# Optimization experiments

Hardware: AMD Instinct MI355X
Metric: run time of the kernel (lower is better)

The kernel has to match this reference:

```python
import jax, jax.numpy as jnp
import numpy as np

B, S, D = 2, 2048, 640
H, DH = 8, 80  # heads, dim_head
SCALE = DH ** -0.5


def setup_inputs() -> dict:
    key = jax.random.key(0)
    ks = jax.random.split(key, 7)
    std = D ** -0.5
    return {
        "x": jax.random.normal(ks[0], (B, S, D), jnp.float32),
        "encoder_hidden_states": jax.random.normal(ks[1], (B, S, D), jnp.float32),
        # Linear weights stored as [in, out] so application is x @ W
        "Wq": jax.random.normal(ks[2], (D, H * DH), jnp.float32) * std,
        "Wk": jax.random.normal(ks[3], (D, H * DH), jnp.float32) * std,
        "Wv": jax.random.normal(ks[4], (D, H * DH), jnp.float32) * std,
        "Wo": jax.random.normal(ks[5], (H * DH, D), jnp.float32) * std,
        "bo": jax.random.normal(ks[6], (D,), jnp.float32) * 0.01,
    }


def reference(x, encoder_hidden_states, Wq, Wk, Wv, Wo, bo):
    # projections (to_q/to_k/to_v have bias=False)
    q = x @ Wq                      # [B, S, H*DH]
    k = encoder_hidden_states @ Wk  # [B, S, H*DH]
    v = encoder_hidden_states @ Wv  # [B, S, H*DH]

    def split_heads(t):
        b, s, _ = t.shape
        return t.reshape(b, s, H, DH).transpose(0, 2, 1, 3)  # [B, H, S, DH]

    q, k, v = split_heads(q), split_heads(k), split_heads(v)

    # the torch loop over bh-chunks computes plain softmax attention; same math fused
    scores = jnp.einsum("bhid,bhjd->bhij", q, k) * SCALE  # [B, H, Sq, Skv]
    attn = jax.nn.softmax(scores, axis=-1)
    out = jnp.einsum("bhij,bhjd->bhid", attn, v)          # [B, H, Sq, DH]

    out = out.transpose(0, 2, 1, 3).reshape(x.shape[0], x.shape[1], H * DH)
    return out @ Wo + bo  # to_out[0]; Dropout(p=0) is identity
```

## Files before the change

kernel.cpp:

```cpp
#include <hip/hip_runtime.h>
#include <hip/hip_bf16.h>

typedef __bf16 v4bf __attribute__((ext_vector_type(4)));
typedef __bf16 v8bf __attribute__((ext_vector_type(8)));
typedef float  v4f  __attribute__((ext_vector_type(4)));

namespace {
constexpr int Bb  = 2;
constexpr int Ss  = 2048;
constexpr int Dd  = 640;
constexpr int Hh  = 8;
constexpr int DHh = 80;
constexpr int Mm  = Bb * Ss;
constexpr float kQScale = 0.11180339887498949f * 1.4426950408889634f;

__device__ __forceinline__ float4 ld4(const float* p) {
  return *reinterpret_cast<const float4*>(p);
}
}

__global__ __launch_bounds__(256)
void wtrans_kernel(const float* __restrict__ Wq, const float* __restrict__ Wk,
                   const float* __restrict__ Wv, const float* __restrict__ Wo,
                   __bf16* __restrict__ Wtq, __bf16* __restrict__ Wtk,
                   __bf16* __restrict__ Wtv, __bf16* __restrict__ Wto) {
  const int z = blockIdx.z;
  const float* W = (z == 0) ? Wq : (z == 1) ? Wk : (z == 2) ? Wv : Wo;
  __bf16* Wt = (z == 0) ? Wtq : (z == 1) ? Wtk : (z == 2) ? Wtv : Wto;
  const int k0 = blockIdx.y * 32, n0 = blockIdx.x * 32;
  __shared__ float t[32][33];
  const int tid = threadIdx.x;
  {
    int kr = tid >> 3, c4 = (tid & 7) * 4;
    float4 f = ld4(W + (size_t)(k0 + kr) * Dd + n0 + c4);
    t[kr][c4 + 0] = f.x; t[kr][c4 + 1] = f.y;
    t[kr][c4 + 2] = f.z; t[kr][c4 + 3] = f.w;
  }
  __syncthreads();
  {
    int nr = tid >> 3, kc = (tid & 7) * 4;
    v4bf p;
#pragma unroll
    for (int u = 0; u < 4; ++u) p[u] = (__bf16)t[kc + u][nr];
    *reinterpret_cast<v4bf*>(&Wt[(size_t)(n0 + nr) * Dd + k0 + kc]) = p;
  }
}

template <bool AF32>
__device__ __forceinline__ void gemm_core_db(const void* __restrict__ Ap,
                                             const __bf16* __restrict__ Bt,
                                             __bf16* As, __bf16* Bs, int m0,
                                             int n0, int rh, int ch,
                                             v4f acc[4][4]) {
  constexpr int BUF = 128 * 40;
  constexpr int NKB = Dd / 32;
  const int tid = threadIdx.x;
  const int lane = tid & 63;
  const int quad = lane >> 4, l15 = lane & 15;
  const int lr = tid >> 1;
  const int lk = (tid & 1) * 16;
  const __bf16* Bg = Bt + (size_t)(n0 + lr) * Dd + lk;
  const float* Af = (const float*)Ap;
  const __bf16* Ab = (const __bf16*)Ap;

#pragma unroll
  for (int i = 0; i < 4; ++i)
#pragma unroll
    for (int j = 0; j < 4; ++j) acc[i][j] = (v4f){0.f, 0.f, 0.f, 0.f};

  v8bf a0, a1, b0, b1;
  if constexpr (AF32) {
    const float* ap = Af + (size_t)(m0 + lr) * Dd + lk;
    float4 f0 = ld4(ap), f1 = ld4(ap + 4), f2 = ld4(ap + 8), f3 = ld4(ap + 12);
    a0[0]=(__bf16)f0.x; a0[1]=(__bf16)f0.y; a0[2]=(__bf16)f0.z; a0[3]=(__bf16)f0.w;
    a0[4]=(__bf16)f1.x; a0[5]=(__bf16)f1.y; a0[6]=(__bf16)f1.z; a0[7]=(__bf16)f1.w;
    a1[0]=(__bf16)f2.x; a1[1]=(__bf16)f2.y; a1[2]=(__bf16)f2.z; a1[3]=(__bf16)f2.w;
    a1[4]=(__bf16)f3.x; a1[5]=(__bf16)f3.y; a1[6]=(__bf16)f3.z; a1[7]=(__bf16)f3.w;
  } else {
    const __bf16* ap = Ab + (size_t)(m0 + lr) * Dd + lk;
    a0 = *reinterpret_cast<const v8bf*>(ap);
    a1 = *reinterpret_cast<const v8bf*>(ap + 8);
  }
  b0 = *reinterpret_cast<const v8bf*>(Bg);
  b1 = *reinterpret_cast<const v8bf*>(Bg + 8);
  *reinterpret_cast<v8bf*>(&As[lr * 40 + lk])     = a0;
  *reinterpret_cast<v8bf*>(&As[lr * 40 + lk + 8]) = a1;
  *reinterpret_cast<v8bf*>(&Bs[lr * 40 + lk])     = b0;
  *reinterpret_cast<v8bf*>(&Bs[lr * 40 + lk + 8]) = b1;

  for (int it = 0; it < NKB; ++it) {
    if (it + 1 < NKB) {
      const int kb = (it + 1) * 32;
      if constexpr (AF32) {
        const float* ap = Af + (size_t)(m0 + lr) * Dd + kb + lk;
        float4 f0 = ld4(ap), f1 = ld4(ap + 4), f2 = ld4(ap + 8),
               f3 = ld4(ap + 12);
        a0[0]=(__bf16)f0.x; a0[1]=(__bf16)f0.y; a0[2]=(__bf16)f0.z; a0[3]=(__bf16)f0.w;
        a0[4]=(__bf16)f1.x; a0[5]=(__bf16)f1.y; a0[6]=(__bf16)f1.z; a0[7]=(__bf16)f1.w;
        a1[0]=(__bf16)f2.x; a1[1]=(__bf16)f2.y; a1[2]=(__bf16)f2.z; a1[3]=(__bf16)f2.w;
        a1[4]=(__bf16)f3.x; a1[5]=(__bf16)f3.y; a1[6]=(__bf16)f3.z; a1[7]=(__bf16)f3.w;
      } else {
        const __bf16* ap = Ab + (size_t)(m0 + lr) * Dd + kb + lk;
        a0 = *reinterpret_cast<const v8bf*>(ap);
        a1 = *reinterpret_cast<const v8bf*>(ap + 8);
      }
      b0 = *reinterpret_cast<const v8bf*>(Bg + kb);
      b1 = *reinterpret_cast<const v8bf*>(Bg + kb + 8);
    }
    __syncthreads();
    const int cur = (it & 1) * BUF, nxt = BUF - cur;
    v8bf af[4], bv[4];
#pragma unroll
    for (int i = 0; i < 4; ++i)
      af[i] = *reinterpret_cast<const v8bf*>(
          &As[cur + (rh + i * 16 + l15) * 40 + quad * 8]);
#pragma unroll
    for (int j = 0; j < 4; ++j)
      bv[j] = *reinterpret_cast<const v8bf*>(
          &Bs[cur + (ch + j * 16 + l15) * 40 + quad * 8]);
#pragma unroll
    for (int i = 0; i < 4; ++i)
#pragma unroll
      for (int j = 0; j < 4; ++j)
        acc[i][j] = __builtin_amdgcn_mfma_f32_16x16x32_bf16(af[i], bv[j],
                                                            acc[i][j], 0, 0, 0);
    if (it + 1 < NKB) {
      *reinterpret_cast<v8bf*>(&As[nxt + lr * 40 + lk])     = a0;
      *reinterpret_cast<v8bf*>(&As[nxt + lr * 40 + lk + 8]) = a1;
      *reinterpret_cast<v8bf*>(&Bs[nxt + lr * 40 + lk])     = b0;
      *reinterpret_cast<v8bf*>(&Bs[nxt + lr * 40 + lk + 8]) = b1;
    }
  }
}

__global__ __launch_bounds__(256)
void gemm_qkv_mfma(const float* __restrict__ x, const float* __restrict__ ehs,
                   const __bf16* __restrict__ Wtq,
                   const __bf16* __restrict__ Wtk,
                   const __bf16* __restrict__ Wtv, __bf16* __restrict__ qb,
                   __bf16* __restrict__ kbuf, __bf16* __restrict__ vb) {
  const int z = blockIdx.z;
  const float* A = (z == 0) ? x : ehs;
  const __bf16* Bt = (z == 0) ? Wtq : (z == 1) ? Wtk : Wtv;
  __bf16* C = (z == 0) ? qb : (z == 1) ? kbuf : vb;
  const float scale = (z == 0) ? kQScale : 1.0f;

  __shared__ __bf16 As[2 * 128 * 40];
  __shared__ __bf16 Bs[2 * 128 * 40];
  const int tid = threadIdx.x;
  const int w = tid >> 6, lane = tid & 63;
  const int quad = lane >> 4, l15 = lane & 15;
  const int m0 = blockIdx.y * 128, n0 = blockIdx.x * 128;
  const int rh = (w >> 1) * 64, ch = (w & 1) * 64;
  v4f acc[4][4];
  gemm_core_db<true>(A, Bt, As, Bs, m0, n0, rh, ch, acc);

  if (z == 2) {
#pragma unroll
    for (int i = 0; i < 4; ++i)
#pragma unroll
      for (int j = 0; j < 4; ++j) {
        int m = m0 + rh + i * 16 + quad * 4;
        int n = n0 + ch + j * 16 + l15;
        int bb = m >> 11, tok = m & 2047;
        v4bf pk;
#pragma unroll
        for (int r = 0; r < 4; ++r) pk[r] = (__bf16)acc[i][j][r];
        *reinterpret_cast<v4bf*>(&C[((size_t)bb * Dd + n) * Ss + tok]) = pk;
      }
  } else {
#pragma unroll
    for (int i = 0; i < 4; ++i)
#pragma unroll
      for (int j = 0; j < 4; ++j) {
        int m = m0 + rh + i * 16 + quad * 4;
        int n = n0 + ch + j * 16 + l15;
#pragma unroll
        for (int r = 0; r < 4; ++r)
          C[(size_t)(m + r) * Dd + n] = (__bf16)(acc[i][j][r] * scale);
      }
  }
}

__global__ __launch_bounds__(256)
void gemm_out_mfma(const __bf16* __restrict__ A, const __bf16* __restrict__ Bt,
                   const float* __restrict__ bias, float* __restrict__ out) {
  __shared__ __bf16 As[2 * 128 * 40];
  __shared__ __bf16 Bs[2 * 128 * 40];
  const int tid = threadIdx.x;
  const int w = tid >> 6, lane = tid & 63;
  const int quad = lane >> 4, l15 = lane & 15;
  const int m0 = blockIdx.y * 128, n0 = blockIdx.x * 128;
  const int rh = (w >> 1) * 64, ch = (w & 1) * 64;
  v4f acc[4][4];
  gemm_core_db<false>(A, Bt, As, Bs, m0, n0, rh, ch, acc);

#pragma unroll
  for (int i = 0; i < 4; ++i)
#pragma unroll
    for (int j = 0; j < 4; ++j) {
      int m = m0 + rh + i * 16 + quad * 4;
      int n = n0 + ch + j * 16 + l15;
      float bn = bias[n];
#pragma unroll
      for (int r = 0; r < 4; ++r)
        out[(size_t)(m + r) * Dd + n] = acc[i][j][r] + bn;
    }
}

__global__ __launch_bounds__(256, 2)
void attn_mfma_kernel(const __bf16* __restrict__ q,
                      const __bf16* __restrict__ k,
                      const __bf16* __restrict__ vtg, __bf16* __restrict__ o) {
  constexpr int QT = 64;
  constexpr int KT = 32;
  constexpr int KW = Ss / 4;
  constexpr int NIT = KW / KT;
  constexpr int LQ = 104;
  constexpr int LV = 40;
  constexpr int KS = KT * LQ;
  constexpr int VS = 96 * LV;
  constexpr int PS = QT * LV;
  constexpr int WSZ = KS + VS + PS;
  constexpr int LM = 100;

  __shared__ __align__(16) __bf16 smem[4 * WSZ];

  const int bh = blockIdx.y;
  const int b = bh >> 3, h = bh & 7;
  const int q0 = blockIdx.x * QT;
  const int tid = threadIdx.x;
  const int w = tid >> 6;
  const int lane = tid & 63;
  const int quad = lane >> 4;
  const int l15 = lane & 15;

  __bf16* ksw = smem + w * WSZ;
  __bf16* vtw = ksw + KS;
  __bf16* psw = vtw + VS;

  const __bf16* qg  = q + (size_t)(b * Ss + q0) * Dd + h * DHh;
  const __bf16* kgb = k + (size_t)(b * Ss) * Dd + h * DHh;
  const __bf16* vgb = vtg + ((size_t)b * Dd + h * DHh) * Ss;

  v8bf qf[4][3];
#pragma unroll
  for (int qt = 0; qt < 4; ++qt)
#pragma unroll
    for (int s = 0; s < 3; ++s) {
      if (s == 2 && quad >= 2) {
        qf[qt][s] = (v8bf){};
      } else {
        qf[qt][s] = *reinterpret_cast<const v8bf*>(
            qg + (size_t)(qt * 16 + l15) * Dd + s * 32 + quad * 8);
      }
    }

  const int kgo = (lane >> 1) * Dd + (lane & 1) * 4;
  const int klo = (lane >> 1) * LQ + (lane & 1) * 4;
  const int vgo = (lane >> 2) * Ss + (lane & 3) * 8;
  const int vlo = (lane >> 2) * LV + (lane & 3) * 8;

  {
    v8bf z8 = {};
    *reinterpret_cast<v8bf*>(&ksw[(lane >> 1) * LQ + 80 + (lane & 1) * 8]) = z8;
    v8bf pad = {};
    int vr = 80 + (lane >> 2);
    if (vr == 80) {
#pragma unroll
      for (int e = 0; e < 8; ++e) pad[e] = (__bf16)1.f;
    }
    *reinterpret_cast<v8bf*>(&vtw[vr * LV + (lane & 3) * 8]) = pad;
  }
  {
    const __bf16* kg = kgb + (size_t)(w * KW) * Dd;
#pragma unroll
    for (int c = 0; c < 10; ++c)
      *reinterpret_cast<v4bf*>(&ksw[klo + c * 8]) =
          *reinterpret_cast<const v4bf*>(kg + kgo + c * 8);
  }

  v4f Oacc[4][6];
#pragma unroll
  for (int qt = 0; qt < 4; ++qt)
#pragma unroll
    for (int mt = 0; mt < 6; ++mt) Oacc[qt][mt] = (v4f){0.f, 0.f, 0.f, 0.f};

  for (int it = 0; it < NIT; ++it) {
    const bool pfK = (it + 1 < NIT);
    v4bf kreg[10];
    if (pfK) {
      const __bf16* kg = kgb + (size_t)(w * KW + (it + 1) * KT) * Dd;
#pragma unroll
      for (int c = 0; c < 10; ++c)
        kreg[c] = *reinterpret_cast<const v4bf*>(kg + kgo + c * 8);
    }

    v4f sacc[4][2];
#pragma unroll
    for (int qt = 0; qt < 4; ++qt) {
      sacc[qt][0] = (v4f){0.f, 0.f, 0.f, 0.f};
      sacc[qt][1] = (v4f){0.f, 0.f, 0.f, 0.f};
    }
    __builtin_amdgcn_s_setprio(1);
#pragma unroll
    for (int s = 0; s < 3; ++s) {
      v8bf ak0 = *reinterpret_cast<const v8bf*>(
          &ksw[l15 * LQ + s * 32 + quad * 8]);
      v8bf ak1 = *reinterpret_cast<const v8bf*>(
          &ksw[(16 + l15) * LQ + s * 32 + quad * 8]);
#pragma unroll
      for (int qt = 0; qt < 4; ++qt) {
        sacc[qt][0] = __builtin_amdgcn_mfma_f32_16x16x32_bf16(
            ak0, qf[qt][s], sacc[qt][0], 0, 0, 0);
        sacc[qt][1] = __builtin_amdgcn_mfma_f32_16x16x32_bf16(
            ak1, qf[qt][s], sacc[qt][1], 0, 0, 0);
      }
    }

    v8bf vreg[5];
    {
      const __bf16* vg = vgb + (w * KW + it * KT);
#pragma unroll
      for (int c = 0; c < 5; ++c)
        vreg[c] = *reinterpret_cast<const v8bf*>(vg + vgo +
                                                 (size_t)c * 16 * Ss);
    }

    if (it > 0) {
      v8bf bp[4];
#pragma unroll
      for (int qt = 0; qt < 4; ++qt)
        bp[qt] = *reinterpret_cast<const v8bf*>(
            &psw[(qt * 16 + l15) * LV + quad * 8]);
#pragma unroll
      for (int mt = 0; mt < 6; ++mt) {
        v8bf av = *reinterpret_cast<const v8bf*>(
            &vtw[(mt * 16 + l15) * LV + quad * 8]);
#pragma unroll
        for (int qt = 0; qt < 4; ++qt)
          Oacc[qt][mt] = __builtin_amdgcn_mfma_f32_16x16x32_bf16(
              av, bp[qt], Oacc[qt][mt], 0, 0, 0);
      }
    }
    __builtin_amdgcn_s_setprio(0);

#pragma unroll
    for (int qt = 0; qt < 4; ++qt)
#pragma unroll
      for (int mt = 0; mt < 2; ++mt) {
        v4bf pk;
#pragma unroll
        for (int r = 0; r < 4; ++r) pk[r] = (__bf16)exp2f(sacc[qt][mt][r]);
        *reinterpret_cast<v4bf*>(
            &psw[(qt * 16 + l15) * LV + mt * 16 + quad * 4]) = pk;
      }

    if (pfK) {
#pragma unroll
      for (int c = 0; c < 10; ++c)
        *reinterpret_cast<v4bf*>(&ksw[klo + c * 8]) = kreg[c];
    }
#pragma unroll
    for (int c = 0; c < 5; ++c)
      *reinterpret_cast<v8bf*>(&vtw[vlo + c * 16 * LV]) = vreg[c];
  }

  {
    v8bf bp[4];
#pragma unroll
    for (int qt = 0; qt < 4; ++qt)
      bp[qt] = *reinterpret_cast<const v8bf*>(
          &psw[(qt * 16 + l15) * LV + quad * 8]);
    __builtin_amdgcn_s_setprio(1);
#pragma unroll
    for (int mt = 0; mt < 6; ++mt) {
      v8bf av = *reinterpret_cast<const v8bf*>(
          &vtw[(mt * 16 + l15) * LV + quad * 8]);
#pragma unroll
      for (int qt = 0; qt < 4; ++qt)
        Oacc[qt][mt] = __builtin_amdgcn_mfma_f32_16x16x32_bf16(
            av, bp[qt], Oacc[qt][mt], 0, 0, 0);
    }
    __builtin_amdgcn_s_setprio(0);
  }

  __syncthreads();
  float* mrg = (float*)smem;
  if (w >= 2) {
    float* base = mrg + (w - 2) * (QT * LM);
#pragma unroll
    for (int qt = 0; qt < 4; ++qt)
#pragma unroll
      for (int mt = 0; mt < 6; ++mt)
        *reinterpret_cast<v4f*>(
            &base[(qt * 16 + l15) * LM + mt * 16 + quad * 4]) = Oacc[qt][mt];
  }
  __syncthreads();
  if (w < 2) {
    const float* base = mrg + w * (QT * LM);
#pragma unroll
    for (int qt = 0; qt < 4; ++qt)
#pragma unroll
      for (int mt = 0; mt < 6; ++mt)
        Oacc[qt][mt] += *reinterpret_cast<const v4f*>(
            &base[(qt * 16 + l15) * LM + mt * 16 + quad * 4]);
  }
  __syncthreads();
  if (w == 1) {
#pragma unroll
    for (int qt = 0; qt < 4; ++qt)
#pragma unroll
      for (int mt = 0; mt < 6; ++mt)
        *reinterpret_cast<v4f*>(
            &mrg[(qt * 16 + l15) * LM + mt * 16 + quad * 4]) = Oacc[qt][mt];
  }
  __syncthreads();
  if (w == 0) {
#pragma unroll
    for (int qt = 0; qt < 4; ++qt)
#pragma unroll
      for (int mt = 0; mt < 6; ++mt)
        Oacc[qt][mt] += *reinterpret_cast<const v4f*>(
            &mrg[(qt * 16 + l15) * LM + mt * 16 + quad * 4]);
#pragma unroll
    for (int qt = 0; qt < 4; ++qt) {
      float lsum = __shfl(Oacc[qt][5][0], l15);
      float inv = 1.f / lsum;
      __bf16* og =
          o + (size_t)(b * Ss + q0 + qt * 16 + l15) * Dd + h * DHh;
#pragma unroll
      for (int mt = 0; mt < 5; ++mt) {
        v4bf pk;
#pragma unroll
        for (int r = 0; r < 4; ++r) pk[r] = (__bf16)(Oacc[qt][mt][r] * inv);
        *reinterpret_cast<v4bf*>(&og[mt * 16 + quad * 4]) = pk;
      }
    }
  }
}

extern "C" void kernel_launch(void* const* d_in, const int* in_sizes, int n_in,
                              void* d_out, int out_size, void* d_ws,
                              size_t ws_size, hipStream_t stream) {
  const float* x   = (const float*)d_in[0];
  const float* ehs = (const float*)d_in[1];
  const float* Wq  = (const float*)d_in[2];
  const float* Wk  = (const float*)d_in[3];
  const float* Wv  = (const float*)d_in[4];
  const float* Wo  = (const float*)d_in[5];
  const float* bo  = (const float*)d_in[6];
  float* out = (float*)d_out;

  __bf16* qb  = (__bf16*)d_ws;
  __bf16* kb  = qb + (size_t)Mm * Dd;
  __bf16* vb  = kb + (size_t)Mm * Dd;
  __bf16* ab  = vb + (size_t)Mm * Dd;
  __bf16* Wtq = ab + (size_t)Mm * Dd;
  __bf16* Wtk = Wtq + (size_t)Dd * Dd;
  __bf16* Wtv = Wtk + (size_t)Dd * Dd;
  __bf16* Wto = Wtv + (size_t)Dd * Dd;

  wtrans_kernel<<<dim3(Dd / 32, Dd / 32, 4), 256, 0, stream>>>(
      Wq, Wk, Wv, Wo, Wtq, Wtk, Wtv, Wto);
  gemm_qkv_mfma<<<dim3(Dd / 128, Mm / 128, 3), 256, 0, stream>>>(
      x, ehs, Wtq, Wtk, Wtv, qb, kb, vb);
  attn_mfma_kernel<<<dim3(Ss / 64, Bb * Hh), 256, 0, stream>>>(qb, kb, vb, ab);
  gemm_out_mfma<<<dim3(Dd / 128, Mm / 128), 256, 0, stream>>>(ab, Wto, bo,
                                                              out);
}
```

Baseline: 156.9 us.

## Stage GEMM tiles with direct global-to-LDS loads and pre-cast activations to bf16

Replaces the register-staged double-buffered GEMM tile loads with global_load_lds (direct global-to-LDS DMA), using an unpadded 32-wide LDS layout. A separate cast kernel converts x and encoder_hidden_states to bf16 up front, so the QKV GEMM can use the same bf16 loader instead of converting fp32 inside the loop. This frees VGPRs and load/store instructions in the main loop. In exchange it adds an extra kernel launch with fp32 read and bf16 write traffic, and the unpadded LDS stride may cause bank conflicts on the MFMA fragment reads.

```diff
diff --git a/kernel.cpp b/kernel.cpp
--- a/kernel.cpp
+++ b/kernel.cpp
@@ -17,6 +17,25 @@
 __device__ __forceinline__ float4 ld4(const float* p) {
   return *reinterpret_cast<const float4*>(p);
 }
+
+__device__ __forceinline__ void gload16(const __bf16* g, __bf16* l) {
+  __builtin_amdgcn_global_load_lds(
+      (const __attribute__((address_space(1))) void*)g,
+      (__attribute__((address_space(3))) void*)l, 16, 0, 0);
+}
+}
+
+__global__ __launch_bounds__(256)
+void cast_kernel(const float* __restrict__ x, const float* __restrict__ ehs,
+                 __bf16* __restrict__ xb, __bf16* __restrict__ eb) {
+  const float* src = (blockIdx.y == 0) ? x : ehs;
+  __bf16* dst = (blockIdx.y == 0) ? xb : eb;
+  size_t idx = ((size_t)blockIdx.x * 256 + threadIdx.x) * 8;
+  float4 f0 = ld4(src + idx), f1 = ld4(src + idx + 4);
+  v8bf p;
+  p[0]=(__bf16)f0.x; p[1]=(__bf16)f0.y; p[2]=(__bf16)f0.z; p[3]=(__bf16)f0.w;
+  p[4]=(__bf16)f1.x; p[5]=(__bf16)f1.y; p[6]=(__bf16)f1.z; p[7]=(__bf16)f1.w;
+  *reinterpret_cast<v8bf*>(&dst[idx]) = p;
 }
 
 __global__ __launch_bounds__(256)
@@ -46,114 +65,88 @@
   }
 }
 
-template <bool AF32>
-__device__ __forceinline__ void gemm_core_db(const void* __restrict__ Ap,
-                                             const __bf16* __restrict__ Bt,
-                                             __bf16* As, __bf16* Bs, int m0,
-                                             int n0, int rh, int ch,
-                                             v4f acc[4][4]) {
-  constexpr int BUF = 128 * 40;
+__device__ __forceinline__ void stage_tile(const __bf16* __restrict__ A,
+                                           const __bf16* __restrict__ Bt,
+                                           __bf16* As, __bf16* Bs, int m0,
+                                           int n0, int kb, int w, int srow,
+                                           int scol) {
+  const __bf16* ga = A + (size_t)(m0 + w * 32 + srow) * Dd + kb + scol;
+  const __bf16* gb = Bt + (size_t)(n0 + w * 32 + srow) * Dd + kb + scol;
+  __bf16* la = As + (w * 32) * 32;
+  __bf16* lb = Bs + (w * 32) * 32;
+#pragma unroll
+  for (int i = 0; i < 2; ++i) {
+    gload16(ga + (size_t)i * 16 * Dd, la + i * 16 * 32);
+    gload16(gb + (size_t)i * 16 * Dd, lb + i * 16 * 32);
+  }
+}
+
+__device__ __forceinline__ void gemm_core_lds(const __bf16* __restrict__ A,
+                                              const __bf16* __restrict__ Bt,
+                                              __bf16* As, __bf16* Bs, int m0,
+                                              int n0, int rh, int ch,
+                                              v4f acc[4][4]) {
+  constexpr int BUF = 128 * 32;
   constexpr int NKB = Dd / 32;
   const int tid = threadIdx.x;
-  const int lane = tid & 63;
+  const int w = tid >> 6, lane = tid & 63;
   const int quad = lane >> 4, l15 = lane & 15;
-  const int lr = tid >> 1;
-  const int lk = (tid & 1) * 16;
-  const __bf16* Bg = Bt + (size_t)(n0 + lr) * Dd + lk;
-  const float* Af = (const float*)Ap;
-  const __bf16* Ab = (const __bf16*)Ap;
+  const int srow = lane >> 2, scol = (lane & 3) * 8;
 
 #pragma unroll
   for (int i = 0; i < 4; ++i)
 #pragma unroll
     for (int j = 0; j < 4; ++j) acc[i][j] = (v4f){0.f, 0.f, 0.f, 0.f};
 
-  v8bf a0, a1, b0, b1;
-  if constexpr (AF32) {
-    const float* ap = Af + (size_t)(m0 + lr) * Dd + lk;
-    float4 f0 = ld4(ap), f1 = ld4(ap + 4), f2 = ld4(ap + 8), f3 = ld4(ap + 12);
-    a0[0]=(__bf16)f0.x; a0[1]=(__bf16)f0.y; a0[2]=(__bf16)f0.z; a0[3]=(__bf16)f0.w;
-    a0[4]=(__bf16)f1.x; a0[5]=(__bf16)f1.y; a0[6]=(__bf16)f1.z; a0[7]=(__bf16)f1.w;
-    a1[0]=(__bf16)f2.x; a1[1]=(__bf16)f2.y; a1[2]=(__bf16)f2.z; a1[3]=(__bf16)f2.w;
-    a1[4]=(__bf16)f3.x; a1[5]=(__bf16)f3.y; a1[6]=(__bf16)f3.z; a1[7]=(__bf16)f3.w;
-  } else {
-    const __bf16* ap = Ab + (size_t)(m0 + lr) * Dd + lk;
-    a0 = *reinterpret_cast<const v8bf*>(ap);
-    a1 = *reinterpret_cast<const v8bf*>(ap + 8);
-  }
-  b0 = *reinterpret_cast<const v8bf*>(Bg);
-  b1 = *reinterpret_cast<const v8bf*>(Bg + 8);
-  *reinterpret_cast<v8bf*>(&As[lr * 40 + lk])     = a0;
-  *reinterpret_cast<v8bf*>(&As[lr * 40 + lk + 8]) = a1;
-  *reinterpret_cast<v8bf*>(&Bs[lr * 40 + lk])     = b0;
-  *reinterpret_cast<v8bf*>(&Bs[lr * 40 + lk + 8]) = b1;
+  stage_tile(A, Bt, As, Bs, m0, n0, 0, w, srow, scol);
 
   for (int it = 0; it < NKB; ++it) {
+    __syncthreads();
     if (it + 1 < NKB) {
-      const int kb = (it + 1) * 32;
-      if constexpr (AF32) {
-        const float* ap = Af + (size_t)(m0 + lr) * Dd + kb + lk;
-        float4 f0 = ld4(ap), f1 = ld4(ap + 4), f2 = ld4(ap + 8),
-               f3 = ld4(ap + 12);
-        a0[0]=(__bf16)f0.x; a0[1]=(__bf16)f0.y; a0[2]=(__bf16)f0.z; a0[3]=(__bf16)f0.w;
-        a0[4]=(__bf16)f1.x; a0[5]=(__bf16)f1.y; a0[6]=(__bf16)f1.z; a0[7]=(__bf16)f1.w;
-        a1[0]=(__bf16)f2.x; a1[1]=(__bf16)f2.y; a1[2]=(__bf16)f2.z; a1[3]=(__bf16)f2.w;
-        a1[4]=(__bf16)f3.x; a1[5]=(__bf16)f3.y; a1[6]=(__bf16)f3.z; a1[7]=(__bf16)f3.w;
-      } else {
-        const __bf16* ap = Ab + (size_t)(m0 + lr) * Dd + kb + lk;
-        a0 = *reinterpret_cast<const v8bf*>(ap);
-        a1 = *reinterpret_cast<const v8bf*>(ap + 8);
-      }
-      b0 = *reinterpret_cast<const v8bf*>(Bg + kb);
-      b1 = *reinterpret_cast<const v8bf*>(Bg + kb + 8);
-    }
-    __syncthreads();
-    const int cur = (it & 1) * BUF, nxt = BUF - cur;
+      const int nb = (it + 1) & 1;
+      stage_tile(A, Bt, As + nb * BUF, Bs + nb * BUF, m0, n0, (it + 1) * 32, w,
+                 srow, scol);
+    }
+    const int cur = (it & 1) * BUF;
     v8bf af[4], bv[4];
 #pragma unroll
     for (int i = 0; i < 4; ++i)
       af[i] = *reinterpret_cast<const v8bf*>(
-          &As[cur + (rh + i * 16 + l15) * 40 + quad * 8]);
+          &As[cur + (rh + i * 16 + l15) * 32 + quad * 8]);
 #pragma unroll
     for (int j = 0; j < 4; ++j)
       bv[j] = *reinterpret_cast<const v8bf*>(
-          &Bs[cur + (ch + j * 16 + l15) * 40 + quad * 8]);
+          &Bs[cur + (ch + j * 16 + l15) * 32 + quad * 8]);
 #pragma unroll
     for (int i = 0; i < 4; ++i)
 #pragma unroll
       for (int j = 0; j < 4; ++j)
         acc[i][j] = __builtin_amdgcn_mfma_f32_16x16x32_bf16(af[i], bv[j],
                                                             acc[i][j], 0, 0, 0);
-    if (it + 1 < NKB) {
-      *reinterpret_cast<v8bf*>(&As[nxt + lr * 40 + lk])     = a0;
-      *reinterpret_cast<v8bf*>(&As[nxt + lr * 40 + lk + 8]) = a1;
-      *reinterpret_cast<v8bf*>(&Bs[nxt + lr * 40 + lk])     = b0;
-      *reinterpret_cast<v8bf*>(&Bs[nxt + lr * 40 + lk + 8]) = b1;
-    }
   }
 }
 
 __global__ __launch_bounds__(256)
-void gemm_qkv_mfma(const float* __restrict__ x, const float* __restrict__ ehs,
+void gemm_qkv_mfma(const __bf16* __restrict__ xb, const __bf16* __restrict__ eb,
                    const __bf16* __restrict__ Wtq,
                    const __bf16* __restrict__ Wtk,
                    const __bf16* __restrict__ Wtv, __bf16* __restrict__ qb,
                    __bf16* __restrict__ kbuf, __bf16* __restrict__ vb) {
   const int z = blockIdx.z;
-  const float* A = (z == 0) ? x : ehs;
+  const __bf16* A = (z == 0) ? xb : eb;
   const __bf16* Bt = (z == 0) ? Wtq : (z == 1) ? Wtk : Wtv;
   __bf16* C = (z == 0) ? qb : (z == 1) ? kbuf : vb;
   const float scale = (z == 0) ? kQScale : 1.0f;
 
-  __shared__ __bf16 As[2 * 128 * 40];
-  __shared__ __bf16 Bs[2 * 128 * 40];
+  __shared__ __align__(16) __bf16 As[2 * 128 * 32];
+  __shared__ __align__(16) __bf16 Bs[2 * 128 * 32];
   const int tid = threadIdx.x;
   const int w = tid >> 6, lane = tid & 63;
   const int quad = lane >> 4, l15 = lane & 15;
   const int m0 = blockIdx.y * 128, n0 = blockIdx.x * 128;
   const int rh = (w >> 1) * 64, ch = (w & 1) * 64;
   v4f acc[4][4];
-  gemm_core_db<true>(A, Bt, As, Bs, m0, n0, rh, ch, acc);
+  gemm_core_lds(A, Bt, As, Bs, m0, n0, rh, ch, acc);
 
   if (z == 2) {
 #pragma unroll
@@ -185,15 +178,15 @@
 __global__ __launch_bounds__(256)
 void gemm_out_mfma(const __bf16* __restrict__ A, const __bf16* __restrict__ Bt,
                    const float* __restrict__ bias, float* __restrict__ out) {
-  __shared__ __bf16 As[2 * 128 * 40];
-  __shared__ __bf16 Bs[2 * 128 * 40];
+  __shared__ __align__(16) __bf16 As[2 * 128 * 32];
+  __shared__ __align__(16) __bf16 Bs[2 * 128 * 32];
   const int tid = threadIdx.x;
   const int w = tid >> 6, lane = tid & 63;
   const int quad = lane >> 4, l15 = lane & 15;
   const int m0 = blockIdx.y * 128, n0 = blockIdx.x * 128;
   const int rh = (w >> 1) * 64, ch = (w & 1) * 64;
   v4f acc[4][4];
-  gemm_core_db<false>(A, Bt, As, Bs, m0, n0, rh, ch, acc);
+  gemm_core_lds(A, Bt, As, Bs, m0, n0, rh, ch, acc);
 
 #pragma unroll
   for (int i = 0; i < 4; ++i)
@@ -460,11 +453,14 @@
   __bf16* Wtk = Wtq + (size_t)Dd * Dd;
   __bf16* Wtv = Wtk + (size_t)Dd * Dd;
   __bf16* Wto = Wtv + (size_t)Dd * Dd;
-
+  __bf16* xb  = Wto + (size_t)Dd * Dd;
+  __bf16* eb  = xb + (size_t)Mm * Dd;
+
+  cast_kernel<<<dim3(Mm * Dd / (256 * 8), 2), 256, 0, stream>>>(x, ehs, xb, eb);
   wtrans_kernel<<<dim3(Dd / 32, Dd / 32, 4), 256, 0, stream>>>(
       Wq, Wk, Wv, Wo, Wtq, Wtk, Wtv, Wto);
   gemm_qkv_mfma<<<dim3(Dd / 128, Mm / 128, 3), 256, 0, stream>>>(
-      x, ehs, Wtq, Wtk, Wtv, qb, kb, vb);
+      xb, eb, Wtq, Wtk, Wtv, qb, kb, vb);
   attn_mfma_kernel<<<dim3(Ss / 64, Bb * Hh), 256, 0, stream>>>(qb, kb, vb, ab);
   gemm_out_mfma<<<dim3(Dd / 128, Mm / 128), 256, 0, stream>>>(ab, Wto, bo,
                                                               out);
```

After: 166.0 us. +5.8%, slower.

## Store Q/K head-major and swap attention grid order for contiguous K loads

Applied to the files above, without the earlier changes.

The QKV GEMM epilogue now writes Q and K in a [B,H,S,DH] head-major layout instead of token-major [B*S,D]. The attention kernel reads K tiles as contiguous 16-byte chunks and scatters them into padded LDS rows through precomputed offsets. The attention grid is also transposed so consecutive blocks cover different heads of the same query tile, which changes L2 reuse across blocks. The GEMM epilogue stores become strided per row, so its write coalescing may suffer.

```diff
diff --git a/kernel.cpp b/kernel.cpp
--- a/kernel.cpp
+++ b/kernel.cpp
@@ -175,9 +175,12 @@
       for (int j = 0; j < 4; ++j) {
         int m = m0 + rh + i * 16 + quad * 4;
         int n = n0 + ch + j * 16 + l15;
+        int hh = n / DHh, d = n % DHh;
+        int bb = m >> 11, tok = m & 2047;
+        __bf16* base = &C[(((size_t)bb * Hh + hh) * Ss + tok) * DHh + d];
 #pragma unroll
         for (int r = 0; r < 4; ++r)
-          C[(size_t)(m + r) * Dd + n] = (__bf16)(acc[i][j][r] * scale);
+          base[(size_t)r * DHh] = (__bf16)(acc[i][j][r] * scale);
       }
   }
 }
@@ -226,9 +229,9 @@
 
   __shared__ __align__(16) __bf16 smem[4 * WSZ];
 
-  const int bh = blockIdx.y;
+  const int bh = blockIdx.x;
   const int b = bh >> 3, h = bh & 7;
-  const int q0 = blockIdx.x * QT;
+  const int q0 = blockIdx.y * QT;
   const int tid = threadIdx.x;
   const int w = tid >> 6;
   const int lane = tid & 63;
@@ -239,8 +242,8 @@
   __bf16* vtw = ksw + KS;
   __bf16* psw = vtw + VS;
 
-  const __bf16* qg  = q + (size_t)(b * Ss + q0) * Dd + h * DHh;
-  const __bf16* kgb = k + (size_t)(b * Ss) * Dd + h * DHh;
+  const __bf16* qg  = q + ((size_t)(b * Hh + h) * Ss + q0) * DHh;
+  const __bf16* kgb = k + (size_t)(b * Hh + h) * Ss * DHh;
   const __bf16* vgb = vtg + ((size_t)b * Dd + h * DHh) * Ss;
 
   v8bf qf[4][3];
@@ -252,12 +255,16 @@
         qf[qt][s] = (v8bf){};
       } else {
         qf[qt][s] = *reinterpret_cast<const v8bf*>(
-            qg + (size_t)(qt * 16 + l15) * Dd + s * 32 + quad * 8);
-      }
-    }
-
-  const int kgo = (lane >> 1) * Dd + (lane & 1) * 4;
-  const int klo = (lane >> 1) * LQ + (lane & 1) * 4;
+            qg + (size_t)(qt * 16 + l15) * DHh + s * 32 + quad * 8);
+      }
+    }
+
+  int klr[5];
+#pragma unroll
+  for (int c = 0; c < 5; ++c) {
+    int E = c * 512 + lane * 8;
+    klr[c] = (E / DHh) * LQ + (E % DHh);
+  }
   const int vgo = (lane >> 2) * Ss + (lane & 3) * 8;
   const int vlo = (lane >> 2) * LV + (lane & 3) * 8;
 
@@ -273,11 +280,11 @@
     *reinterpret_cast<v8bf*>(&vtw[vr * LV + (lane & 3) * 8]) = pad;
   }
   {
-    const __bf16* kg = kgb + (size_t)(w * KW) * Dd;
-#pragma unroll
-    for (int c = 0; c < 10; ++c)
-      *reinterpret_cast<v4bf*>(&ksw[klo + c * 8]) =
-          *reinterpret_cast<const v4bf*>(kg + kgo + c * 8);
+    const __bf16* kg = kgb + (size_t)(w * KW) * DHh;
+#pragma unroll
+    for (int c = 0; c < 5; ++c)
+      *reinterpret_cast<v8bf*>(&ksw[klr[c]]) =
+          *reinterpret_cast<const v8bf*>(kg + c * 512 + lane * 8);
   }
 
   v4f Oacc[4][6];
@@ -288,12 +295,12 @@
 
   for (int it = 0; it < NIT; ++it) {
     const bool pfK = (it + 1 < NIT);
-    v4bf kreg[10];
+    v8bf kreg[5];
     if (pfK) {
-      const __bf16* kg = kgb + (size_t)(w * KW + (it + 1) * KT) * Dd;
-#pragma unroll
-      for (int c = 0; c < 10; ++c)
-        kreg[c] = *reinterpret_cast<const v4bf*>(kg + kgo + c * 8);
+      const __bf16* kg = kgb + (size_t)(w * KW + (it + 1) * KT) * DHh;
+#pragma unroll
+      for (int c = 0; c < 5; ++c)
+        kreg[c] = *reinterpret_cast<const v8bf*>(kg + c * 512 + lane * 8);
     }
 
     v4f sacc[4][2];
@@ -358,8 +365,8 @@
 
     if (pfK) {
 #pragma unroll
-      for (int c = 0; c < 10; ++c)
-        *reinterpret_cast<v4bf*>(&ksw[klo + c * 8]) = kreg[c];
+      for (int c = 0; c < 5; ++c)
+        *reinterpret_cast<v8bf*>(&ksw[klr[c]]) = kreg[c];
     }
 #pragma unroll
     for (int c = 0; c < 5; ++c)
@@ -465,7 +472,7 @@
       Wq, Wk, Wv, Wo, Wtq, Wtk, Wtv, Wto);
   gemm_qkv_mfma<<<dim3(Dd / 128, Mm / 128, 3), 256, 0, stream>>>(
       x, ehs, Wtq, Wtk, Wtv, qb, kb, vb);
-  attn_mfma_kernel<<<dim3(Ss / 64, Bb * Hh), 256, 0, stream>>>(qb, kb, vb, ab);
+  attn_mfma_kernel<<<dim3(Bb * Hh, Ss / 64), 256, 0, stream>>>(qb, kb, vb, ab);
   gemm_out_mfma<<<dim3(Dd / 128, Mm / 128), 256, 0, stream>>>(ab, Wto, bo,
                                                               out);
 }
```

Result: no change. 155.8 us (-0.7%).
